# Optimization experiments

Hardware: AMD Instinct MI355X
Metric: run time of the kernel (lower is better)

The kernel has to match this reference:

```python
import jax, jax.numpy as jnp
import numpy as np

HIDDEN = 2048
INTER = 5632
NCODES = 4096
VEC = 8
TOKENS = 4096


def dequant(codebook, idx, scale):
    # codebook: [NCODES, VEC]; idx: [out, in//VEC] int32; scale: [out]
    out, ncol = idx.shape
    w = codebook[idx].reshape(out, ncol * VEC)  # [out, in]
    return w * scale[:, None]


def setup_inputs() -> dict:
    key = jax.random.key(0)
    ks = jax.random.split(key, 10)
    return {
        "x": jax.random.normal(ks[0], (TOKENS, HIDDEN), dtype=jnp.float32),
        "codebook_gate": jax.random.normal(ks[1], (NCODES, VEC), dtype=jnp.float32),
        "idx_gate": jax.random.randint(ks[2], (INTER, HIDDEN // VEC), 0, NCODES, dtype=jnp.int32),
        "scale_gate": jax.random.uniform(ks[3], (INTER,), dtype=jnp.float32, minval=0.01, maxval=0.05),
        "codebook_up": jax.random.normal(ks[4], (NCODES, VEC), dtype=jnp.float32),
        "idx_up": jax.random.randint(ks[5], (INTER, HIDDEN // VEC), 0, NCODES, dtype=jnp.int32),
        "scale_up": jax.random.uniform(ks[6], (INTER,), dtype=jnp.float32, minval=0.01, maxval=0.05),
        "codebook_down": jax.random.normal(ks[7], (NCODES, VEC), dtype=jnp.float32),
        "idx_down": jax.random.randint(ks[8], (HIDDEN, INTER // VEC), 0, NCODES, dtype=jnp.int32),
        "scale_down": jax.random.uniform(ks[9], (HIDDEN,), dtype=jnp.float32, minval=0.01, maxval=0.05),
    }


def reference(x, codebook_gate, idx_gate, scale_gate,
              codebook_up, idx_up, scale_up,
              codebook_down, idx_down, scale_down):
    # Dequantize trellis/codebook weights, then SwiGLU:
    # out = down( silu(gate(x)) * up(x) )
    w_gate = dequant(codebook_gate, idx_gate, scale_gate)  # [INTER, HIDDEN]
    w_up = dequant(codebook_up, idx_up, scale_up)          # [INTER, HIDDEN]
    w_down = dequant(codebook_down, idx_down, scale_down)  # [HIDDEN, INTER]
    gate = jax.nn.silu(x @ w_gate.T)                       # [T, INTER]
    up = x @ w_up.T                                        # [T, INTER]
    return (gate * up) @ w_down.T                          # [T, HIDDEN]
```

## Files before the change

### kernel.cpp

```cpp
#include <hip/hip_runtime.h>

#define HIDDEN 2048
#define INTER  5632
#define TOKENS 4096

#define BM 128
#define BN 128
#define BK 64
#define GROUP_N 4

#define BM1 256
#define BN1 128
#define NT1 (HIDDEN / BK)

using bf16x8 = __attribute__((ext_vector_type(8))) __bf16;
using f32x4  = __attribute__((ext_vector_type(4))) float;

__device__ __forceinline__ unsigned short f2bf(float f) {
    unsigned int u = __float_as_uint(f);
    u += 0x7FFFu + ((u >> 16) & 1u);
    return (unsigned short)(u >> 16);
}

#define GLDS(gptr, lptr) \
    __builtin_amdgcn_global_load_lds((__attribute__((address_space(1))) void*)(gptr), \
                                     (__attribute__((address_space(3))) void*)(lptr), 16, 0, 0)

__global__ __launch_bounds__(512) void prep_kernel(
        const float* __restrict__ x, unsigned short* __restrict__ xb,
        const int* __restrict__ ig, const float* __restrict__ cbg,
        const float* __restrict__ sg, unsigned short* __restrict__ wg,
        const int* __restrict__ iu, const float* __restrict__ cbu,
        const float* __restrict__ su, unsigned short* __restrict__ wu,
        const int* __restrict__ idn, const float* __restrict__ cbd,
        const float* __restrict__ sd, unsigned short* __restrict__ wd) {
    __shared__ unsigned short cbl[4096 * 8];
    const int b = blockIdx.x;
    const int tid = threadIdx.x;

    if (b >= 528) {
        int t = (b - 528) * 512 + tid;
        const float4* x4 = (const float4*)x;
        float4 a = x4[2 * t];
        float4 c = x4[2 * t + 1];
        uint4 o;
        o.x = f2bf(a.x) | ((unsigned int)f2bf(a.y) << 16);
        o.y = f2bf(a.z) | ((unsigned int)f2bf(a.w) << 16);
        o.z = f2bf(c.x) | ((unsigned int)f2bf(c.y) << 16);
        o.w = f2bf(c.z) | ((unsigned int)f2bf(c.w) << 16);
        ((uint4*)xb)[t] = o;
        return;
    }

    const int mat = b / 176;
    const int bl  = b % 176;
    const int* idx; const float* cb; const float* scale; unsigned short* w; int ncol8;
    if (mat == 0)      { idx = ig;  cb = cbg; scale = sg; w = wg; ncol8 = HIDDEN / 8; }
    else if (mat == 1) { idx = iu;  cb = cbu; scale = su; w = wu; ncol8 = HIDDEN / 8; }
    else               { idx = idn; cb = cbd; scale = sd; w = wd; ncol8 = INTER / 8; }

#pragma unroll
    for (int i = 0; i < 8; ++i) {
        int r = i * 512 + tid;
        const float4* c4 = (const float4*)(cb + ((size_t)r << 3));
        float4 a = c4[0];
        float4 c = c4[1];
        uint4 o;
        o.x = f2bf(a.x) | ((unsigned int)f2bf(a.y) << 16);
        o.y = f2bf(a.z) | ((unsigned int)f2bf(a.w) << 16);
        o.z = f2bf(c.x) | ((unsigned int)f2bf(c.y) << 16);
        o.w = f2bf(c.z) | ((unsigned int)f2bf(c.w) << 16);
        ((uint4*)cbl)[r] = o;
    }
    __syncthreads();

    const size_t base = (size_t)bl * 8192;
#pragma unroll 2
    for (int i = 0; i < 16; ++i) {
        size_t t = base + i * 512 + tid;
        int id = idx[t];
        float s = scale[t / ncol8];
        const unsigned short* cw = cbl + ((unsigned)id << 3);
        uint4 cv = *(const uint4*)cw;
        unsigned int ww[4];
#pragma unroll
        for (int j = 0; j < 4; ++j) {
            unsigned int pair = (&cv.x)[j];
            float lo = __uint_as_float(pair << 16) * s;
            float hi = __uint_as_float(pair & 0xFFFF0000u) * s;
            ww[j] = f2bf(lo) | ((unsigned int)f2bf(hi) << 16);
        }
        uint4 o = {ww[0], ww[1], ww[2], ww[3]};
        ((uint4*)w)[t] = o;
    }
}

__device__ __forceinline__ void decode_block(int bid, int nblocks_m, int nblocks_n,
                                             int* mb, int* nb) {
    int gw = nblocks_m * GROUP_N;
    int group = bid / gw;
    int inb = bid % gw;
    int gn = group * GROUP_N;
    int width = (nblocks_n - gn < GROUP_N) ? (nblocks_n - gn) : GROUP_N;
    *mb = inb / width;
    *nb = gn + inb % width;
}

__global__ __launch_bounds__(512, 2) void gemm1_kernel(const unsigned short* __restrict__ X,
                                                       const unsigned short* __restrict__ Wg,
                                                       const unsigned short* __restrict__ Wu,
                                                       unsigned short* __restrict__ H) {
    __shared__ unsigned short As[2][BM1 * BK];
    __shared__ unsigned short Bgs[2][BN1 * BK];
    __shared__ unsigned short Bus[2][BN1 * BK];

    const int tid  = threadIdx.x;
    const int lane = tid & 63;
    const int wave = tid >> 6;
    int mb, nb;
    decode_block(blockIdx.x, TOKENS / BM1, INTER / BN1, &mb, &nb);
    const int m0 = mb * BM1;
    const int n0 = nb * BN1;

    const int srow = tid >> 3;
    const int scol = (tid & 7) << 3;
    const int gcol = (((tid & 7) ^ (srow & 7))) << 3;

    const int wr = wave >> 1;
    const int wc = wave & 1;
    const int ln15 = lane & 15;
    const int lq = lane >> 4;
    const int swr = ln15 & 7;

    f32x4 accg[4][4], accu[4][4];
    const f32x4 z = {0.f, 0.f, 0.f, 0.f};
    for (int i = 0; i < 4; ++i)
        for (int j = 0; j < 4; ++j) { accg[i][j] = z; accu[i][j] = z; }

#define STAGE1(buf, kt) do {                                                        \
        const int k0_ = (kt) * BK;                                                  \
        _Pragma("unroll")                                                           \
        for (int i_ = 0; i_ < 4; ++i_) {                                            \
            const int r_ = i_ * 64 + srow;                                          \
            GLDS(X + (size_t)(m0 + r_) * HIDDEN + k0_ + gcol,                       \
                 &As[buf][r_ * BK + scol]);                                         \
        }                                                                           \
        _Pragma("unroll")                                                           \
        for (int i_ = 0; i_ < 2; ++i_) {                                            \
            const int r_ = i_ * 64 + srow;                                          \
            GLDS(Wg + (size_t)(n0 + r_) * HIDDEN + k0_ + gcol,                      \
                 &Bgs[buf][r_ * BK + scol]);                                        \
            GLDS(Wu + (size_t)(n0 + r_) * HIDDEN + k0_ + gcol,                      \
                 &Bus[buf][r_ * BK + scol]);                                        \
        }                                                                           \
    } while (0)

    STAGE1(0, 0);
    STAGE1(1, 1);
    asm volatile("s_waitcnt vmcnt(8)" ::: "memory");
    __builtin_amdgcn_s_barrier();

    for (int t = 0; t < NT1; ++t) {
        const int cur = t & 1;
        bf16x8 af[4], bg[4], bu[4];
#pragma unroll
        for (int ks = 0; ks < 2; ++ks) {
            const int pofs = (((ks * 4 + lq) ^ swr)) << 3;
#pragma unroll
            for (int im = 0; im < 4; ++im)
                af[im] = *(const bf16x8*)(&As[cur][(wr * 64 + im * 16 + ln15) * BK + pofs]);
#pragma unroll
            for (int in = 0; in < 4; ++in)
                bg[in] = *(const bf16x8*)(&Bgs[cur][(wc * 64 + in * 16 + ln15) * BK + pofs]);
            __builtin_amdgcn_s_barrier();
            asm volatile("s_waitcnt lgkmcnt(0)" ::: "memory");
            __builtin_amdgcn_s_setprio(1);
#pragma unroll
            for (int im = 0; im < 4; ++im)
#pragma unroll
                for (int in = 0; in < 4; ++in)
                    accg[im][in] = __builtin_amdgcn_mfma_f32_16x16x32_bf16(af[im], bg[in], accg[im][in], 0, 0, 0);
            __builtin_amdgcn_s_setprio(0);
            __builtin_amdgcn_s_barrier();
#pragma unroll
            for (int in = 0; in < 4; ++in)
                bu[in] = *(const bf16x8*)(&Bus[cur][(wc * 64 + in * 16 + ln15) * BK + pofs]);
            __builtin_amdgcn_s_barrier();
            asm volatile("s_waitcnt lgkmcnt(0)" ::: "memory");
            __builtin_amdgcn_s_setprio(1);
#pragma unroll
            for (int im = 0; im < 4; ++im)
#pragma unroll
                for (int in = 0; in < 4; ++in)
                    accu[im][in] = __builtin_amdgcn_mfma_f32_16x16x32_bf16(af[im], bu[in], accu[im][in], 0, 0, 0);
            __builtin_amdgcn_s_setprio(0);
            __builtin_amdgcn_s_barrier();
        }
        if (t + 2 < NT1) {
            STAGE1(cur, t + 2);
            asm volatile("s_waitcnt vmcnt(8)" ::: "memory");
            __builtin_amdgcn_s_barrier();
        } else if (t + 1 < NT1) {
            asm volatile("s_waitcnt vmcnt(0)" ::: "memory");
            __builtin_amdgcn_s_barrier();
        }
    }
#undef STAGE1

#pragma unroll
    for (int im = 0; im < 4; ++im)
#pragma unroll
        for (int in = 0; in < 4; ++in) {
            const int row = m0 + wr * 64 + im * 16 + lq * 4;
            const int col = n0 + wc * 64 + in * 16 + ln15;
#pragma unroll
            for (int r = 0; r < 4; ++r) {
                float g = accg[im][in][r];
                float u = accu[im][in][r];
                float h = g * (1.0f / (1.0f + __expf(-g))) * u;
                H[(size_t)(row + r) * INTER + col] = f2bf(h);
            }
        }
}

__global__ __launch_bounds__(256, 3) void gemm2_kernel(const unsigned short* __restrict__ Hin,
                                                       const unsigned short* __restrict__ Wd,
                                                       float* __restrict__ Out) {
    __shared__ unsigned short As[BM * BK];
    __shared__ unsigned short Bs[BN * BK];

    const int tid  = threadIdx.x;
    const int lane = tid & 63;
    const int wave = tid >> 6;
    int mb, nb;
    decode_block(blockIdx.x, TOKENS / BM, HIDDEN / BN, &mb, &nb);
    const int m0 = mb * BM;
    const int n0 = nb * BN;

    const int srow = tid >> 3;
    const int scol = (tid & 7) << 3;
    const int gcol = (((tid & 7) ^ (srow & 7))) << 3;

    const int wr = wave >> 1;
    const int wc = wave & 1;
    const int ln15 = lane & 15;
    const int lq = lane >> 4;
    const int swr = ln15 & 7;

    f32x4 acc[4][4];
    const f32x4 z = {0.f, 0.f, 0.f, 0.f};
    for (int i = 0; i < 4; ++i)
        for (int j = 0; j < 4; ++j) acc[i][j] = z;

    for (int kt = 0; kt < INTER / BK; ++kt) {
        const int k0 = kt * BK;
        __syncthreads();
#pragma unroll
        for (int i = 0; i < 4; ++i) {
            const int r = i * 32 + srow;
            GLDS(Hin + (size_t)(m0 + r) * INTER + k0 + gcol, As + r * BK + scol);
            GLDS(Wd  + (size_t)(n0 + r) * INTER + k0 + gcol, Bs + r * BK + scol);
        }
        __syncthreads();
#pragma unroll
        for (int ks = 0; ks < 2; ++ks) {
            bf16x8 af[4], bf[4];
            const int pofs = (((ks * 4 + lq) ^ swr)) << 3;
#pragma unroll
            for (int im = 0; im < 4; ++im)
                af[im] = *(const bf16x8*)(As + (wr * 64 + im * 16 + ln15) * BK + pofs);
#pragma unroll
            for (int in = 0; in < 4; ++in)
                bf[in] = *(const bf16x8*)(Bs + (wc * 64 + in * 16 + ln15) * BK + pofs);
#pragma unroll
            for (int im = 0; im < 4; ++im)
#pragma unroll
                for (int in = 0; in < 4; ++in)
                    acc[im][in] = __builtin_amdgcn_mfma_f32_16x16x32_bf16(af[im], bf[in], acc[im][in], 0, 0, 0);
        }
    }

#pragma unroll
    for (int im = 0; im < 4; ++im)
#pragma unroll
        for (int in = 0; in < 4; ++in) {
            const int row = m0 + wr * 64 + im * 16 + lq * 4;
            const int col = n0 + wc * 64 + in * 16 + ln15;
#pragma unroll
            for (int r = 0; r < 4; ++r)
                Out[(size_t)(row + r) * HIDDEN + col] = acc[im][in][r];
        }
}

extern "C" void kernel_launch(void* const* d_in, const int* in_sizes, int n_in,
                              void* d_out, int out_size, void* d_ws, size_t ws_size,
                              hipStream_t stream) {
    (void)in_sizes; (void)n_in; (void)out_size; (void)ws_size;

    const float* x   = (const float*)d_in[0];
    const float* cbg = (const float*)d_in[1];
    const int*   ig  = (const int*)d_in[2];
    const float* sg  = (const float*)d_in[3];
    const float* cbu = (const float*)d_in[4];
    const int*   iu  = (const int*)d_in[5];
    const float* su  = (const float*)d_in[6];
    const float* cbd = (const float*)d_in[7];
    const int*   idn = (const int*)d_in[8];
    const float* sd  = (const float*)d_in[9];
    float* out = (float*)d_out;

    char* p = (char*)d_ws;
    unsigned short* Xb = (unsigned short*)p; p += (size_t)TOKENS * HIDDEN * 2;
    unsigned short* Wg = (unsigned short*)p; p += (size_t)INTER * HIDDEN * 2;
    unsigned short* Wu = (unsigned short*)p; p += (size_t)INTER * HIDDEN * 2;
    unsigned short* Wd = (unsigned short*)p; p += (size_t)HIDDEN * INTER * 2;
    unsigned short* H  = (unsigned short*)p; p += (size_t)TOKENS * INTER * 2;

    prep_kernel<<<dim3(528 + 2048), dim3(512), 0, stream>>>(
        x, Xb, ig, cbg, sg, Wg, iu, cbu, su, Wu, idn, cbd, sd, Wd);

    gemm1_kernel<<<dim3((TOKENS / BM1) * (INTER / BN1)), dim3(512), 0, stream>>>(Xb, Wg, Wu, H);
    gemm2_kernel<<<dim3((TOKENS / BM) * (HIDDEN / BN)), dim3(256), 0, stream>>>(H, Wd, out);
}
```

Measured before the change: 420.9 us.

## Simplify gemm1 pipeline and double-buffer gemm2 with larger 256x128 tiles

Gemm1 drops its hand-tuned two-stage prefetch, the split barriers and the setprio ping-pong. It now uses a simple prefetch-next-tile-then-compute scheme with one __syncthreads per K step, and interleaves the gate and up MFMAs. Gemm2 moves to 512-thread blocks with 256x128 tiles and a double-buffered LDS prefetch of the next K tile, meant to cut global-load stalls and raise per-block reuse. The larger gemm2 tile halves the grid to 256 blocks, which may underfill the CUs. The simplified gemm1 may also lose the overlap the old schedule gave.

```diff
diff --git a/kernel.cpp b/kernel.cpp
--- a/kernel.cpp
+++ b/kernel.cpp
@@ -4,14 +4,16 @@
 #define INTER  5632
 #define TOKENS 4096
 
-#define BM 128
-#define BN 128
 #define BK 64
 #define GROUP_N 4
 
 #define BM1 256
 #define BN1 128
 #define NT1 (HIDDEN / BK)
+
+#define BM2 256
+#define BN2 128
+#define NT2 (INTER / BK)
 
 using bf16x8 = __attribute__((ext_vector_type(8))) __bf16;
 using f32x4  = __attribute__((ext_vector_type(4))) float;
@@ -156,54 +158,32 @@
     } while (0)
 
     STAGE1(0, 0);
-    STAGE1(1, 1);
-    asm volatile("s_waitcnt vmcnt(8)" ::: "memory");
-    __builtin_amdgcn_s_barrier();
+    __syncthreads();
 
     for (int t = 0; t < NT1; ++t) {
         const int cur = t & 1;
-        bf16x8 af[4], bg[4], bu[4];
+        if (t + 1 < NT1) STAGE1(cur ^ 1, t + 1);
 #pragma unroll
         for (int ks = 0; ks < 2; ++ks) {
             const int pofs = (((ks * 4 + lq) ^ swr)) << 3;
+            bf16x8 af[4], bg[4], bu[4];
 #pragma unroll
             for (int im = 0; im < 4; ++im)
                 af[im] = *(const bf16x8*)(&As[cur][(wr * 64 + im * 16 + ln15) * BK + pofs]);
 #pragma unroll
-            for (int in = 0; in < 4; ++in)
+            for (int in = 0; in < 4; ++in) {
                 bg[in] = *(const bf16x8*)(&Bgs[cur][(wc * 64 + in * 16 + ln15) * BK + pofs]);
-            __builtin_amdgcn_s_barrier();
-            asm volatile("s_waitcnt lgkmcnt(0)" ::: "memory");
-            __builtin_amdgcn_s_setprio(1);
+                bu[in] = *(const bf16x8*)(&Bus[cur][(wc * 64 + in * 16 + ln15) * BK + pofs]);
+            }
 #pragma unroll
             for (int im = 0; im < 4; ++im)
 #pragma unroll
-                for (int in = 0; in < 4; ++in)
+                for (int in = 0; in < 4; ++in) {
                     accg[im][in] = __builtin_amdgcn_mfma_f32_16x16x32_bf16(af[im], bg[in], accg[im][in], 0, 0, 0);
-            __builtin_amdgcn_s_setprio(0);
-            __builtin_amdgcn_s_barrier();
-#pragma unroll
-            for (int in = 0; in < 4; ++in)
-                bu[in] = *(const bf16x8*)(&Bus[cur][(wc * 64 + in * 16 + ln15) * BK + pofs]);
-            __builtin_amdgcn_s_barrier();
-            asm volatile("s_waitcnt lgkmcnt(0)" ::: "memory");
-            __builtin_amdgcn_s_setprio(1);
-#pragma unroll
-            for (int im = 0; im < 4; ++im)
-#pragma unroll
-                for (int in = 0; in < 4; ++in)
                     accu[im][in] = __builtin_amdgcn_mfma_f32_16x16x32_bf16(af[im], bu[in], accu[im][in], 0, 0, 0);
-            __builtin_amdgcn_s_setprio(0);
-            __builtin_amdgcn_s_barrier();
-        }
-        if (t + 2 < NT1) {
-            STAGE1(cur, t + 2);
-            asm volatile("s_waitcnt vmcnt(8)" ::: "memory");
-            __builtin_amdgcn_s_barrier();
-        } else if (t + 1 < NT1) {
-            asm volatile("s_waitcnt vmcnt(0)" ::: "memory");
-            __builtin_amdgcn_s_barrier();
-        }
+                }
+        }
+        __syncthreads();
     }
 #undef STAGE1
 
@@ -223,19 +203,19 @@
         }
 }
 
-__global__ __launch_bounds__(256, 3) void gemm2_kernel(const unsigned short* __restrict__ Hin,
+__global__ __launch_bounds__(512, 2) void gemm2_kernel(const unsigned short* __restrict__ Hin,
                                                        const unsigned short* __restrict__ Wd,
                                                        float* __restrict__ Out) {
-    __shared__ unsigned short As[BM * BK];
-    __shared__ unsigned short Bs[BN * BK];
+    __shared__ unsigned short As[2][BM2 * BK];
+    __shared__ unsigned short Bs[2][BN2 * BK];
 
     const int tid  = threadIdx.x;
     const int lane = tid & 63;
     const int wave = tid >> 6;
     int mb, nb;
-    decode_block(blockIdx.x, TOKENS / BM, HIDDEN / BN, &mb, &nb);
-    const int m0 = mb * BM;
-    const int n0 = nb * BN;
+    decode_block(blockIdx.x, TOKENS / BM2, HIDDEN / BN2, &mb, &nb);
+    const int m0 = mb * BM2;
+    const int n0 = nb * BN2;
 
     const int srow = tid >> 3;
     const int scol = (tid & 7) << 3;
@@ -252,33 +232,47 @@
     for (int i = 0; i < 4; ++i)
         for (int j = 0; j < 4; ++j) acc[i][j] = z;
 
-    for (int kt = 0; kt < INTER / BK; ++kt) {
-        const int k0 = kt * BK;
-        __syncthreads();
-#pragma unroll
-        for (int i = 0; i < 4; ++i) {
-            const int r = i * 32 + srow;
-            GLDS(Hin + (size_t)(m0 + r) * INTER + k0 + gcol, As + r * BK + scol);
-            GLDS(Wd  + (size_t)(n0 + r) * INTER + k0 + gcol, Bs + r * BK + scol);
-        }
-        __syncthreads();
+#define STAGE2(buf, kt) do {                                                        \
+        const int k0_ = (kt) * BK;                                                  \
+        _Pragma("unroll")                                                           \
+        for (int i_ = 0; i_ < 4; ++i_) {                                            \
+            const int r_ = i_ * 64 + srow;                                          \
+            GLDS(Hin + (size_t)(m0 + r_) * INTER + k0_ + gcol,                      \
+                 &As[buf][r_ * BK + scol]);                                         \
+        }                                                                           \
+        _Pragma("unroll")                                                           \
+        for (int i_ = 0; i_ < 2; ++i_) {                                            \
+            const int r_ = i_ * 64 + srow;                                          \
+            GLDS(Wd + (size_t)(n0 + r_) * INTER + k0_ + gcol,                       \
+                 &Bs[buf][r_ * BK + scol]);                                         \
+        }                                                                           \
+    } while (0)
+
+    STAGE2(0, 0);
+    __syncthreads();
+
+    for (int t = 0; t < NT2; ++t) {
+        const int cur = t & 1;
+        if (t + 1 < NT2) STAGE2(cur ^ 1, t + 1);
 #pragma unroll
         for (int ks = 0; ks < 2; ++ks) {
+            const int pofs = (((ks * 4 + lq) ^ swr)) << 3;
             bf16x8 af[4], bf[4];
-            const int pofs = (((ks * 4 + lq) ^ swr)) << 3;
 #pragma unroll
             for (int im = 0; im < 4; ++im)
-                af[im] = *(const bf16x8*)(As + (wr * 64 + im * 16 + ln15) * BK + pofs);
+                af[im] = *(const bf16x8*)(&As[cur][(wr * 64 + im * 16 + ln15) * BK + pofs]);
 #pragma unroll
             for (int in = 0; in < 4; ++in)
-                bf[in] = *(const bf16x8*)(Bs + (wc * 64 + in * 16 + ln15) * BK + pofs);
+                bf[in] = *(const bf16x8*)(&Bs[cur][(wc * 64 + in * 16 + ln15) * BK + pofs]);
 #pragma unroll
             for (int im = 0; im < 4; ++im)
 #pragma unroll
                 for (int in = 0; in < 4; ++in)
                     acc[im][in] = __builtin_amdgcn_mfma_f32_16x16x32_bf16(af[im], bf[in], acc[im][in], 0, 0, 0);
         }
-    }
+        __syncthreads();
+    }
+#undef STAGE2
 
 #pragma unroll
     for (int im = 0; im < 4; ++im)
@@ -320,5 +314,5 @@
         x, Xb, ig, cbg, sg, Wg, iu, cbu, su, Wu, idn, cbd, sd, Wd);
 
     gemm1_kernel<<<dim3((TOKENS / BM1) * (INTER / BN1)), dim3(512), 0, stream>>>(Xb, Wg, Wu, H);
-    gemm2_kernel<<<dim3((TOKENS / BM) * (HIDDEN / BN)), dim3(256), 0, stream>>>(H, Wd, out);
-}
+    gemm2_kernel<<<dim3((TOKENS / BM2) * (HIDDEN / BN2)), dim3(512), 0, stream>>>(H, Wd, out);
+}
```

Measured after the change: 426.2 us. About the same (+1.3%).
